# Performance work log

Measured on AMD Instinct MI355X. Metric: run time of the kernel, lower is better.

Reference implementation:

```python
import jax, jax.numpy as jnp
import numpy as np

B, NQ, NK, DQ, DK, H, DV = 4, 128, 1024, 256, 256, 256, 256
MASK_VAL = -1e6


def setup_inputs() -> dict:
    key = jax.random.key(0)
    ks = jax.random.split(key, 7)
    queries = jax.random.normal(ks[0], (B, NQ, DQ), dtype=jnp.float32)
    keys = jax.random.normal(ks[1], (B, NK, DK), dtype=jnp.float32)
    values = jax.random.normal(ks[2], (B, NK, DV), dtype=jnp.float32)
    # per-batch valid lengths in [1, NK]
    valid_lens = jax.random.randint(ks[3], (B,), 1, NK + 1, dtype=jnp.int64 if jax.config.read('jax_enable_x64') else jnp.int32)
    W_q = jax.random.normal(ks[4], (DQ, H), dtype=jnp.float32) * (1.0 / np.sqrt(DQ))
    W_k = jax.random.normal(ks[5], (DK, H), dtype=jnp.float32) * (1.0 / np.sqrt(DK))
    v_w = jax.random.normal(ks[6], (H,), dtype=jnp.float32) * (1.0 / np.sqrt(H))
    return {"queries": queries, "keys": keys, "values": values,
            "valid_lens": valid_lens, "W_q": W_q, "W_k": W_k, "v_w": v_w}


def reference(queries, keys, values, valid_lens, W_q, W_k, v_w):
    # Project queries and keys to the shared hidden space.
    q = jnp.einsum('bqd,dh->bqh', queries, W_q)          # (B, NQ, H)
    k = jnp.einsum('bkd,dh->bkh', keys, W_k)             # (B, NK, H)
    # Broadcast-add + tanh -> (B, NQ, NK, H), then contract with v to scores.
    features = jnp.tanh(q[:, :, None, :] + k[:, None, :, :])
    scores = jnp.einsum('bqkh,h->bqk', features, v_w)    # (B, NQ, NK)
    # Masked softmax over the key axis: positions >= valid_len get -1e6.
    nk = scores.shape[-1]
    mask = jnp.arange(nk)[None, None, :] < valid_lens[:, None, None]
    scores = jnp.where(mask, scores, MASK_VAL)
    attention_weights = jax.nn.softmax(scores, axis=-1)
    # Weighted sum of values (bmm).
    return jnp.einsum('bqk,bkv->bqv', attention_weights, values)
```

## Files before the change

kernel.cpp:

```cpp
#include <hip/hip_runtime.h>

#define B_   4
#define NQ_  128
#define NK_  1024
#define DD_  256
#define H_   256
#define DV_  256

__device__ __forceinline__ float wave_sum(float v) {
  #pragma unroll
  for (int o = 32; o; o >>= 1) v += __shfl_xor(v, o);
  return v;
}
__device__ __forceinline__ float wave_max(float v) {
  #pragma unroll
  for (int o = 32; o; o >>= 1) v = fmaxf(v, __shfl_xor(v, o));
  return v;
}

__global__ __launch_bounds__(256) void proj_merged_kernel(
    const float* __restrict__ queries, const float* __restrict__ keys,
    const float* __restrict__ W_q, const float* __restrict__ W_k,
    float* __restrict__ qp, float* __restrict__ kpT) {
  __shared__ float As[16 * 36];
  __shared__ float Ws[16 * 68];
  __shared__ float Ts[64 * 36];
  const int tid  = threadIdx.x;
  const int row0 = blockIdx.x * 32;
  const int col0 = blockIdx.y * 64;
  const bool isQ = row0 < 512;
  const float* A = isQ ? queries + (size_t)row0 * DD_
                       : keys + (size_t)(row0 - 512) * DD_;
  const float* W = isQ ? W_q : W_k;
  const int ld_d = tid & 15, ld_r = tid >> 4;
  const int lw_n = tid & 63, lw_k = tid >> 6;
  const int tn = tid & 15, tm = tid >> 4;

  float aP[2], wP[4];
  #pragma unroll
  for (int p = 0; p < 2; ++p) aP[p] = A[(size_t)(p * 16 + ld_r) * DD_ + ld_d];
  #pragma unroll
  for (int p = 0; p < 4; ++p) wP[p] = W[(size_t)(p * 4 + lw_k) * H_ + col0 + lw_n];

  float acc[2][4] = {};
  for (int kt = 0; kt < 16; ++kt) {
    __syncthreads();
    #pragma unroll
    for (int p = 0; p < 2; ++p) As[ld_d * 36 + p * 16 + ld_r] = aP[p];
    #pragma unroll
    for (int p = 0; p < 4; ++p) Ws[(p * 4 + lw_k) * 68 + lw_n] = wP[p];
    __syncthreads();
    if (kt < 15) {
      const int k0 = (kt + 1) * 16;
      #pragma unroll
      for (int p = 0; p < 2; ++p) aP[p] = A[(size_t)(p * 16 + ld_r) * DD_ + k0 + ld_d];
      #pragma unroll
      for (int p = 0; p < 4; ++p) wP[p] = W[(size_t)(k0 + p * 4 + lw_k) * H_ + col0 + lw_n];
    }
    #pragma unroll
    for (int kk = 0; kk < 16; ++kk) {
      const float2 a = *(const float2*)&As[kk * 36 + tm * 2];
      const float4 w = *(const float4*)&Ws[kk * 68 + tn * 4];
      acc[0][0] = fmaf(a.x, w.x, acc[0][0]);
      acc[0][1] = fmaf(a.x, w.y, acc[0][1]);
      acc[0][2] = fmaf(a.x, w.z, acc[0][2]);
      acc[0][3] = fmaf(a.x, w.w, acc[0][3]);
      acc[1][0] = fmaf(a.y, w.x, acc[1][0]);
      acc[1][1] = fmaf(a.y, w.y, acc[1][1]);
      acc[1][2] = fmaf(a.y, w.z, acc[1][2]);
      acc[1][3] = fmaf(a.y, w.w, acc[1][3]);
    }
  }

  if (isQ) {
    #pragma unroll
    for (int i = 0; i < 2; ++i) {
      *(float4*)&qp[(size_t)(row0 + tm * 2 + i) * H_ + col0 + tn * 4] =
          make_float4(acc[i][0], acc[i][1], acc[i][2], acc[i][3]);
    }
  } else {
    #pragma unroll
    for (int i = 0; i < 2; ++i)
      #pragma unroll
      for (int j = 0; j < 4; ++j)
        Ts[(tn * 4 + j) * 36 + tm * 2 + i] = acc[i][j];
    __syncthreads();
    const int keyrow = row0 - 512;
    const int b = keyrow >> 10;
    const int kbase = keyrow & (NK_ - 1);
    const int hh = tid >> 2;
    const int kg = (tid & 3) * 8;
    float* dst = kpT + ((size_t)(b * H_ + col0 + hh)) * NK_ + kbase + kg;
    #pragma unroll
    for (int p = 0; p < 2; ++p)
      *(float4*)&dst[p * 4] = *(const float4*)&Ts[hh * 36 + kg + p * 4];
  }
}

__global__ __launch_bounds__(512) void fused_attn_kernel(
    const float* __restrict__ qp, const float* __restrict__ kpT,
    const float* __restrict__ v_w, const float* __restrict__ values,
    const int* __restrict__ valid_lens, float* __restrict__ out) {
  __shared__ float2 qs2[H_];
  __shared__ float w2s[H_];
  __shared__ float reds[4];
  __shared__ float s_half[2][2][NK_];
  __shared__ float redm[2][4];
  __shared__ float redsum[2][4];
  __shared__ float red[8][2][DV_];

  const int tid = threadIdx.x;
  const int n = blockIdx.x;
  const int xcd = n & 7;
  const int b = xcd >> 1;
  const int idx = ((n >> 3) << 1) | (xcd & 1);
  const int qrow = b * NQ_ + idx * 2;

  int vl = valid_lens[b];
  vl = vl < 1 ? 1 : (vl > NK_ ? NK_ : vl);

  const float C2 = 2.8853900817779268f;
  if (tid < H_) {
    const float vw = v_w[tid];
    w2s[tid] = 2.0f * vw;
    const float q0 = qp[(size_t)qrow * H_ + tid];
    const float q1 = qp[(size_t)(qrow + 1) * H_ + tid];
    qs2[tid] = make_float2(q0 * C2, q1 * C2);
    float s = wave_sum(vw);
    if ((tid & 63) == 0) reds[tid >> 6] = s;
  }
  __syncthreads();
  const float wsum = reds[0] + reds[1] + reds[2] + reds[3];

  const int g = tid >> 8;
  const int k0 = (tid & 255) * 4;
  if (k0 < vl) {
    float a0x = 0.f, a0y = 0.f, a0z = 0.f, a0w = 0.f;
    float a1x = 0.f, a1y = 0.f, a1z = 0.f, a1w = 0.f;
    const float* kp = kpT + ((size_t)(b * H_ + g * 128)) * NK_ + k0;
    const float* w2p = w2s + g * 128;
    const float2* q2p = qs2 + g * 128;
    float4 c0 = *(const float4*)(kp + 0 * (size_t)NK_);
    float4 c1 = *(const float4*)(kp + 1 * (size_t)NK_);
    float4 c2 = *(const float4*)(kp + 2 * (size_t)NK_);
    float4 c3 = *(const float4*)(kp + 3 * (size_t)NK_);
#define CONSUME(kv, h)                                                     \
    {                                                                      \
      const float w2 = w2p[h];                                             \
      const float2 q2 = q2p[h];                                            \
      const float e0x = __builtin_amdgcn_exp2f(fmaf((kv).x, C2, q2.x));    \
      const float e0y = __builtin_amdgcn_exp2f(fmaf((kv).y, C2, q2.x));    \
      const float e0z = __builtin_amdgcn_exp2f(fmaf((kv).z, C2, q2.x));    \
      const float e0w = __builtin_amdgcn_exp2f(fmaf((kv).w, C2, q2.x));    \
      const float e1x = __builtin_amdgcn_exp2f(fmaf((kv).x, C2, q2.y));    \
      const float e1y = __builtin_amdgcn_exp2f(fmaf((kv).y, C2, q2.y));    \
      const float e1z = __builtin_amdgcn_exp2f(fmaf((kv).z, C2, q2.y));    \
      const float e1w = __builtin_amdgcn_exp2f(fmaf((kv).w, C2, q2.y));    \
      a0x = fmaf(w2, __builtin_amdgcn_rcpf(1.0f + e0x), a0x);              \
      a0y = fmaf(w2, __builtin_amdgcn_rcpf(1.0f + e0y), a0y);              \
      a0z = fmaf(w2, __builtin_amdgcn_rcpf(1.0f + e0z), a0z);              \
      a0w = fmaf(w2, __builtin_amdgcn_rcpf(1.0f + e0w), a0w);              \
      a1x = fmaf(w2, __builtin_amdgcn_rcpf(1.0f + e1x), a1x);              \
      a1y = fmaf(w2, __builtin_amdgcn_rcpf(1.0f + e1y), a1y);              \
      a1z = fmaf(w2, __builtin_amdgcn_rcpf(1.0f + e1z), a1z);              \
      a1w = fmaf(w2, __builtin_amdgcn_rcpf(1.0f + e1w), a1w);              \
    }
    for (int gg = 0; gg < 31; ++gg) {
      const int hb = gg * 4;
      const float4 n0 = *(const float4*)(kp + (size_t)(hb + 4) * NK_);
      const float4 n1 = *(const float4*)(kp + (size_t)(hb + 5) * NK_);
      const float4 n2 = *(const float4*)(kp + (size_t)(hb + 6) * NK_);
      const float4 n3 = *(const float4*)(kp + (size_t)(hb + 7) * NK_);
      CONSUME(c0, hb + 0)
      CONSUME(c1, hb + 1)
      CONSUME(c2, hb + 2)
      CONSUME(c3, hb + 3)
      c0 = n0; c1 = n1; c2 = n2; c3 = n3;
    }
    CONSUME(c0, 124)
    CONSUME(c1, 125)
    CONSUME(c2, 126)
    CONSUME(c3, 127)
#undef CONSUME
    *(float4*)&s_half[g][0][k0] = make_float4(a0x, a0y, a0z, a0w);
    *(float4*)&s_half[g][1][k0] = make_float4(a1x, a1y, a1z, a1w);
  }
  __syncthreads();

  const int qi = tid >> 8;
  const int k4 = (tid & 255) * 4;
  const float4 pA = *(const float4*)&s_half[0][qi][k4];
  const float4 pB = *(const float4*)&s_half[1][qi][k4];
  const float s0 = wsum - (pA.x + pB.x);
  const float s1 = wsum - (pA.y + pB.y);
  const float s2 = wsum - (pA.z + pB.z);
  const float s3 = wsum - (pA.w + pB.w);
  const float NEG = -3.0e38f;
  float m = NEG;
  m = fmaxf(m, (k4 + 0 < vl) ? s0 : NEG);
  m = fmaxf(m, (k4 + 1 < vl) ? s1 : NEG);
  m = fmaxf(m, (k4 + 2 < vl) ? s2 : NEG);
  m = fmaxf(m, (k4 + 3 < vl) ? s3 : NEG);
  m = wave_max(m);
  if ((tid & 63) == 0) redm[qi][(tid >> 6) & 3] = m;
  __syncthreads();
  const float M = fmaxf(fmaxf(redm[qi][0], redm[qi][1]),
                        fmaxf(redm[qi][2], redm[qi][3]));
  const float CE = 1.4426950408889634f;
  const float p0 = (k4 + 0 < vl) ? __builtin_amdgcn_exp2f((s0 - M) * CE) : 0.0f;
  const float p1 = (k4 + 1 < vl) ? __builtin_amdgcn_exp2f((s1 - M) * CE) : 0.0f;
  const float p2 = (k4 + 2 < vl) ? __builtin_amdgcn_exp2f((s2 - M) * CE) : 0.0f;
  const float p3 = (k4 + 3 < vl) ? __builtin_amdgcn_exp2f((s3 - M) * CE) : 0.0f;
  float psum = wave_sum(p0 + p1 + p2 + p3);
  if ((tid & 63) == 0) redsum[qi][(tid >> 6) & 3] = psum;
  __syncthreads();
  const float S = redsum[qi][0] + redsum[qi][1] + redsum[qi][2] + redsum[qi][3];
  const float inv = 1.0f / S;
  *(float4*)&s_half[0][qi][k4] = make_float4(p0 * inv, p1 * inv, p2 * inv, p3 * inv);
  __syncthreads();

  const int w = tid >> 6;
  const int lane = tid & 63;
  const int d0 = lane * 4;
  float4 pa0 = make_float4(0.f, 0.f, 0.f, 0.f);
  float4 pa1 = make_float4(0.f, 0.f, 0.f, 0.f);
  const int kbeg = w * (NK_ / 8);
  const int kend = (kbeg + NK_ / 8) < vl ? (kbeg + NK_ / 8) : vl;
  const float* vb = values + (size_t)b * NK_ * DV_ + d0;
#define PVSTEP(v4, kk)                                                     \
    {                                                                      \
      const float w0 = s_half[0][0][kk];                                   \
      const float w1 = s_half[0][1][kk];                                   \
      pa0.x = fmaf(w0, (v4).x, pa0.x);                                     \
      pa0.y = fmaf(w0, (v4).y, pa0.y);                                     \
      pa0.z = fmaf(w0, (v4).z, pa0.z);                                     \
      pa0.w = fmaf(w0, (v4).w, pa0.w);                                     \
      pa1.x = fmaf(w1, (v4).x, pa1.x);                                     \
      pa1.y = fmaf(w1, (v4).y, pa1.y);                                     \
      pa1.z = fmaf(w1, (v4).z, pa1.z);                                     \
      pa1.w = fmaf(w1, (v4).w, pa1.w);                                     \
    }
  int k = kbeg;
  if (k + 4 <= kend) {
    float4 v0 = *(const float4*)(vb + (size_t)(k + 0) * DV_);
    float4 v1 = *(const float4*)(vb + (size_t)(k + 1) * DV_);
    float4 v2 = *(const float4*)(vb + (size_t)(k + 2) * DV_);
    float4 v3 = *(const float4*)(vb + (size_t)(k + 3) * DV_);
    for (; k + 8 <= kend; k += 4) {
      const float4 u0 = *(const float4*)(vb + (size_t)(k + 4) * DV_);
      const float4 u1 = *(const float4*)(vb + (size_t)(k + 5) * DV_);
      const float4 u2 = *(const float4*)(vb + (size_t)(k + 6) * DV_);
      const float4 u3 = *(const float4*)(vb + (size_t)(k + 7) * DV_);
      PVSTEP(v0, k + 0)
      PVSTEP(v1, k + 1)
      PVSTEP(v2, k + 2)
      PVSTEP(v3, k + 3)
      v0 = u0; v1 = u1; v2 = u2; v3 = u3;
    }
    PVSTEP(v0, k + 0)
    PVSTEP(v1, k + 1)
    PVSTEP(v2, k + 2)
    PVSTEP(v3, k + 3)
    k += 4;
  }
  for (; k < kend; ++k) {
    const float4 v4 = *(const float4*)(vb + (size_t)k * DV_);
    PVSTEP(v4, k)
  }
#undef PVSTEP
  *(float4*)&red[w][0][d0] = pa0;
  *(float4*)&red[w][1][d0] = pa1;
  __syncthreads();

  const int oqi = tid >> 8;
  const int d = tid & 255;
  float s = 0.f;
  #pragma unroll
  for (int ww = 0; ww < 8; ++ww) s += red[ww][oqi][d];
  out[(size_t)(qrow + oqi) * DV_ + d] = s;
}

extern "C" void kernel_launch(void* const* d_in, const int* in_sizes, int n_in,
                              void* d_out, int out_size, void* d_ws, size_t ws_size,
                              hipStream_t stream) {
  const float* queries = (const float*)d_in[0];
  const float* keys    = (const float*)d_in[1];
  const float* values  = (const float*)d_in[2];
  const int*   vlens   = (const int*)d_in[3];
  const float* W_q     = (const float*)d_in[4];
  const float* W_k     = (const float*)d_in[5];
  const float* v_w     = (const float*)d_in[6];
  float* out = (float*)d_out;

  float* qp  = (float*)d_ws;
  float* kpT = qp + (size_t)B_ * NQ_ * H_;

  proj_merged_kernel<<<dim3((512 + B_ * NK_) / 32, H_ / 64), 256, 0, stream>>>(
      queries, keys, W_q, W_k, qp, kpT);
  fused_attn_kernel<<<(B_ * NQ_) / 2, 512, 0, stream>>>(qp, kpT, v_w, values, vlens, out);
}
```

Before: 123.5 us.

## Process one query per attention block and deepen projection K-tile

```diff
diff --git a/kernel.cpp b/kernel.cpp
--- a/kernel.cpp
+++ b/kernel.cpp
@@ -22,8 +22,8 @@
     const float* __restrict__ queries, const float* __restrict__ keys,
     const float* __restrict__ W_q, const float* __restrict__ W_k,
     float* __restrict__ qp, float* __restrict__ kpT) {
-  __shared__ float As[16 * 36];
-  __shared__ float Ws[16 * 68];
+  __shared__ float As[32 * 36];
+  __shared__ float Ws[32 * 68];
   __shared__ float Ts[64 * 36];
   const int tid  = threadIdx.x;
   const int row0 = blockIdx.x * 32;
@@ -32,33 +32,33 @@
   const float* A = isQ ? queries + (size_t)row0 * DD_
                        : keys + (size_t)(row0 - 512) * DD_;
   const float* W = isQ ? W_q : W_k;
-  const int ld_d = tid & 15, ld_r = tid >> 4;
+  const int ld_d = tid & 31, ld_r = tid >> 5;
   const int lw_n = tid & 63, lw_k = tid >> 6;
   const int tn = tid & 15, tm = tid >> 4;
 
-  float aP[2], wP[4];
-  #pragma unroll
-  for (int p = 0; p < 2; ++p) aP[p] = A[(size_t)(p * 16 + ld_r) * DD_ + ld_d];
-  #pragma unroll
-  for (int p = 0; p < 4; ++p) wP[p] = W[(size_t)(p * 4 + lw_k) * H_ + col0 + lw_n];
+  float aP[4], wP[8];
+  #pragma unroll
+  for (int p = 0; p < 4; ++p) aP[p] = A[(size_t)(p * 8 + ld_r) * DD_ + ld_d];
+  #pragma unroll
+  for (int p = 0; p < 8; ++p) wP[p] = W[(size_t)(p * 4 + lw_k) * H_ + col0 + lw_n];
 
   float acc[2][4] = {};
-  for (int kt = 0; kt < 16; ++kt) {
+  for (int kt = 0; kt < 8; ++kt) {
     __syncthreads();
     #pragma unroll
-    for (int p = 0; p < 2; ++p) As[ld_d * 36 + p * 16 + ld_r] = aP[p];
-    #pragma unroll
-    for (int p = 0; p < 4; ++p) Ws[(p * 4 + lw_k) * 68 + lw_n] = wP[p];
+    for (int p = 0; p < 4; ++p) As[ld_d * 36 + p * 8 + ld_r] = aP[p];
+    #pragma unroll
+    for (int p = 0; p < 8; ++p) Ws[(p * 4 + lw_k) * 68 + lw_n] = wP[p];
     __syncthreads();
-    if (kt < 15) {
-      const int k0 = (kt + 1) * 16;
+    if (kt < 7) {
+      const int k0 = (kt + 1) * 32;
       #pragma unroll
-      for (int p = 0; p < 2; ++p) aP[p] = A[(size_t)(p * 16 + ld_r) * DD_ + k0 + ld_d];
+      for (int p = 0; p < 4; ++p) aP[p] = A[(size_t)(p * 8 + ld_r) * DD_ + k0 + ld_d];
       #pragma unroll
-      for (int p = 0; p < 4; ++p) wP[p] = W[(size_t)(k0 + p * 4 + lw_k) * H_ + col0 + lw_n];
-    }
-    #pragma unroll
-    for (int kk = 0; kk < 16; ++kk) {
+      for (int p = 0; p < 8; ++p) wP[p] = W[(size_t)(k0 + p * 4 + lw_k) * H_ + col0 + lw_n];
+    }
+    #pragma unroll
+    for (int kk = 0; kk < 32; ++kk) {
       const float2 a = *(const float2*)&As[kk * 36 + tm * 2];
       const float4 w = *(const float4*)&Ws[kk * 68 + tn * 4];
       acc[0][0] = fmaf(a.x, w.x, acc[0][0]);
@@ -97,75 +97,61 @@
   }
 }
 
-__global__ __launch_bounds__(512) void fused_attn_kernel(
+__global__ __launch_bounds__(256) void fused_attn_kernel(
     const float* __restrict__ qp, const float* __restrict__ kpT,
     const float* __restrict__ v_w, const float* __restrict__ values,
     const int* __restrict__ valid_lens, float* __restrict__ out) {
-  __shared__ float2 qs2[H_];
+  __shared__ float qs[H_];
   __shared__ float w2s[H_];
   __shared__ float reds[4];
-  __shared__ float s_half[2][2][NK_];
-  __shared__ float redm[2][4];
-  __shared__ float redsum[2][4];
-  __shared__ float red[8][2][DV_];
+  __shared__ float wlds[NK_];
+  __shared__ float redm[4];
+  __shared__ float redsum[4];
+  __shared__ float red[4][DV_];
 
   const int tid = threadIdx.x;
   const int n = blockIdx.x;
   const int xcd = n & 7;
   const int b = xcd >> 1;
   const int idx = ((n >> 3) << 1) | (xcd & 1);
-  const int qrow = b * NQ_ + idx * 2;
+  const int qrow = b * NQ_ + idx;
 
   int vl = valid_lens[b];
   vl = vl < 1 ? 1 : (vl > NK_ ? NK_ : vl);
 
   const float C2 = 2.8853900817779268f;
-  if (tid < H_) {
+  {
     const float vw = v_w[tid];
     w2s[tid] = 2.0f * vw;
-    const float q0 = qp[(size_t)qrow * H_ + tid];
-    const float q1 = qp[(size_t)(qrow + 1) * H_ + tid];
-    qs2[tid] = make_float2(q0 * C2, q1 * C2);
+    qs[tid] = qp[(size_t)qrow * H_ + tid] * C2;
     float s = wave_sum(vw);
     if ((tid & 63) == 0) reds[tid >> 6] = s;
   }
   __syncthreads();
   const float wsum = reds[0] + reds[1] + reds[2] + reds[3];
 
-  const int g = tid >> 8;
-  const int k0 = (tid & 255) * 4;
+  const int k0 = tid * 4;
+  float ax = 0.f, ay = 0.f, az = 0.f, aw = 0.f;
   if (k0 < vl) {
-    float a0x = 0.f, a0y = 0.f, a0z = 0.f, a0w = 0.f;
-    float a1x = 0.f, a1y = 0.f, a1z = 0.f, a1w = 0.f;
-    const float* kp = kpT + ((size_t)(b * H_ + g * 128)) * NK_ + k0;
-    const float* w2p = w2s + g * 128;
-    const float2* q2p = qs2 + g * 128;
+    const float* kp = kpT + ((size_t)(b * H_)) * NK_ + k0;
     float4 c0 = *(const float4*)(kp + 0 * (size_t)NK_);
     float4 c1 = *(const float4*)(kp + 1 * (size_t)NK_);
     float4 c2 = *(const float4*)(kp + 2 * (size_t)NK_);
     float4 c3 = *(const float4*)(kp + 3 * (size_t)NK_);
 #define CONSUME(kv, h)                                                     \
     {                                                                      \
-      const float w2 = w2p[h];                                             \
-      const float2 q2 = q2p[h];                                            \
-      const float e0x = __builtin_amdgcn_exp2f(fmaf((kv).x, C2, q2.x));    \
-      const float e0y = __builtin_amdgcn_exp2f(fmaf((kv).y, C2, q2.x));    \
-      const float e0z = __builtin_amdgcn_exp2f(fmaf((kv).z, C2, q2.x));    \
-      const float e0w = __builtin_amdgcn_exp2f(fmaf((kv).w, C2, q2.x));    \
-      const float e1x = __builtin_amdgcn_exp2f(fmaf((kv).x, C2, q2.y));    \
-      const float e1y = __builtin_amdgcn_exp2f(fmaf((kv).y, C2, q2.y));    \
-      const float e1z = __builtin_amdgcn_exp2f(fmaf((kv).z, C2, q2.y));    \
-      const float e1w = __builtin_amdgcn_exp2f(fmaf((kv).w, C2, q2.y));    \
-      a0x = fmaf(w2, __builtin_amdgcn_rcpf(1.0f + e0x), a0x);              \
-      a0y = fmaf(w2, __builtin_amdgcn_rcpf(1.0f + e0y), a0y);              \
-      a0z = fmaf(w2, __builtin_amdgcn_rcpf(1.0f + e0z), a0z);              \
-      a0w = fmaf(w2, __builtin_amdgcn_rcpf(1.0f + e0w), a0w);              \
-      a1x = fmaf(w2, __builtin_amdgcn_rcpf(1.0f + e1x), a1x);              \
-      a1y = fmaf(w2, __builtin_amdgcn_rcpf(1.0f + e1y), a1y);              \
-      a1z = fmaf(w2, __builtin_amdgcn_rcpf(1.0f + e1z), a1z);              \
-      a1w = fmaf(w2, __builtin_amdgcn_rcpf(1.0f + e1w), a1w);              \
-    }
-    for (int gg = 0; gg < 31; ++gg) {
+      const float w2 = w2s[h];                                             \
+      const float qc = qs[h];                                              \
+      const float ex = __builtin_amdgcn_exp2f(fmaf((kv).x, C2, qc));       \
+      const float ey = __builtin_amdgcn_exp2f(fmaf((kv).y, C2, qc));       \
+      const float ez = __builtin_amdgcn_exp2f(fmaf((kv).z, C2, qc));       \
+      const float ew = __builtin_amdgcn_exp2f(fmaf((kv).w, C2, qc));       \
+      ax = fmaf(w2, __builtin_amdgcn_rcpf(1.0f + ex), ax);                 \
+      ay = fmaf(w2, __builtin_amdgcn_rcpf(1.0f + ey), ay);                 \
+      az = fmaf(w2, __builtin_amdgcn_rcpf(1.0f + ez), az);                 \
+      aw = fmaf(w2, __builtin_amdgcn_rcpf(1.0f + ew), aw);                 \
+    }
+    for (int gg = 0; gg < 63; ++gg) {
       const int hb = gg * 4;
       const float4 n0 = *(const float4*)(kp + (size_t)(hb + 4) * NK_);
       const float4 n1 = *(const float4*)(kp + (size_t)(hb + 5) * NK_);
@@ -177,68 +163,54 @@
       CONSUME(c3, hb + 3)
       c0 = n0; c1 = n1; c2 = n2; c3 = n3;
     }
-    CONSUME(c0, 124)
-    CONSUME(c1, 125)
-    CONSUME(c2, 126)
-    CONSUME(c3, 127)
+    CONSUME(c0, 252)
+    CONSUME(c1, 253)
+    CONSUME(c2, 254)
+    CONSUME(c3, 255)
 #undef CONSUME
-    *(float4*)&s_half[g][0][k0] = make_float4(a0x, a0y, a0z, a0w);
-    *(float4*)&s_half[g][1][k0] = make_float4(a1x, a1y, a1z, a1w);
-  }
-  __syncthreads();
-
-  const int qi = tid >> 8;
-  const int k4 = (tid & 255) * 4;
-  const float4 pA = *(const float4*)&s_half[0][qi][k4];
-  const float4 pB = *(const float4*)&s_half[1][qi][k4];
-  const float s0 = wsum - (pA.x + pB.x);
-  const float s1 = wsum - (pA.y + pB.y);
-  const float s2 = wsum - (pA.z + pB.z);
-  const float s3 = wsum - (pA.w + pB.w);
+  }
+  const float s0 = wsum - ax;
+  const float s1 = wsum - ay;
+  const float s2 = wsum - az;
+  const float s3 = wsum - aw;
+
   const float NEG = -3.0e38f;
   float m = NEG;
-  m = fmaxf(m, (k4 + 0 < vl) ? s0 : NEG);
-  m = fmaxf(m, (k4 + 1 < vl) ? s1 : NEG);
-  m = fmaxf(m, (k4 + 2 < vl) ? s2 : NEG);
-  m = fmaxf(m, (k4 + 3 < vl) ? s3 : NEG);
+  m = fmaxf(m, (k0 + 0 < vl) ? s0 : NEG);
+  m = fmaxf(m, (k0 + 1 < vl) ? s1 : NEG);
+  m = fmaxf(m, (k0 + 2 < vl) ? s2 : NEG);
+  m = fmaxf(m, (k0 + 3 < vl) ? s3 : NEG);
   m = wave_max(m);
-  if ((tid & 63) == 0) redm[qi][(tid >> 6) & 3] = m;
-  __syncthreads();
-  const float M = fmaxf(fmaxf(redm[qi][0], redm[qi][1]),
-                        fmaxf(redm[qi][2], redm[qi][3]));
+  if ((tid & 63) == 0) redm[tid >> 6] = m;
+  __syncthreads();
+  const float M = fmaxf(fmaxf(redm[0], redm[1]), fmaxf(redm[2], redm[3]));
   const float CE = 1.4426950408889634f;
-  const float p0 = (k4 + 0 < vl) ? __builtin_amdgcn_exp2f((s0 - M) * CE) : 0.0f;
-  const float p1 = (k4 + 1 < vl) ? __builtin_amdgcn_exp2f((s1 - M) * CE) : 0.0f;
-  const float p2 = (k4 + 2 < vl) ? __builtin_amdgcn_exp2f((s2 - M) * CE) : 0.0f;
-  const float p3 = (k4 + 3 < vl) ? __builtin_amdgcn_exp2f((s3 - M) * CE) : 0.0f;
+  const float p0 = (k0 + 0 < vl) ? __builtin_amdgcn_exp2f((s0 - M) * CE) : 0.0f;
+  const float p1 = (k0 + 1 < vl) ? __builtin_amdgcn_exp2f((s1 - M) * CE) : 0.0f;
+  const float p2 = (k0 + 2 < vl) ? __builtin_amdgcn_exp2f((s2 - M) * CE) : 0.0f;
+  const float p3 = (k0 + 3 < vl) ? __builtin_amdgcn_exp2f((s3 - M) * CE) : 0.0f;
   float psum = wave_sum(p0 + p1 + p2 + p3);
-  if ((tid & 63) == 0) redsum[qi][(tid >> 6) & 3] = psum;
-  __syncthreads();
-  const float S = redsum[qi][0] + redsum[qi][1] + redsum[qi][2] + redsum[qi][3];
+  if ((tid & 63) == 0) redsum[tid >> 6] = psum;
+  __syncthreads();
+  const float S = redsum[0] + redsum[1] + redsum[2] + redsum[3];
   const float inv = 1.0f / S;
-  *(float4*)&s_half[0][qi][k4] = make_float4(p0 * inv, p1 * inv, p2 * inv, p3 * inv);
+  *(float4*)&wlds[k0] = make_float4(p0 * inv, p1 * inv, p2 * inv, p3 * inv);
   __syncthreads();
 
   const int w = tid >> 6;
   const int lane = tid & 63;
   const int d0 = lane * 4;
-  float4 pa0 = make_float4(0.f, 0.f, 0.f, 0.f);
-  float4 pa1 = make_float4(0.f, 0.f, 0.f, 0.f);
-  const int kbeg = w * (NK_ / 8);
-  const int kend = (kbeg + NK_ / 8) < vl ? (kbeg + NK_ / 8) : vl;
+  float4 pa = make_float4(0.f, 0.f, 0.f, 0.f);
+  const int kbeg = w * (NK_ / 4);
+  const int kend = (kbeg + NK_ / 4) < vl ? (kbeg + NK_ / 4) : vl;
   const float* vb = values + (size_t)b * NK_ * DV_ + d0;
 #define PVSTEP(v4, kk)                                                     \
     {                                                                      \
-      const float w0 = s_half[0][0][kk];                                   \
-      const float w1 = s_half[0][1][kk];                                   \
-      pa0.x = fmaf(w0, (v4).x, pa0.x);                                     \
-      pa0.y = fmaf(w0, (v4).y, pa0.y);                                     \
-      pa0.z = fmaf(w0, (v4).z, pa0.z);                                     \
-      pa0.w = fmaf(w0, (v4).w, pa0.w);                                     \
-      pa1.x = fmaf(w1, (v4).x, pa1.x);                                     \
-      pa1.y = fmaf(w1, (v4).y, pa1.y);                                     \
-      pa1.z = fmaf(w1, (v4).z, pa1.z);                                     \
-      pa1.w = fmaf(w1, (v4).w, pa1.w);                                     \
+      const float w0 = wlds[kk];                                           \
+      pa.x = fmaf(w0, (v4).x, pa.x);                                       \
+      pa.y = fmaf(w0, (v4).y, pa.y);                                       \
+      pa.z = fmaf(w0, (v4).z, pa.z);                                       \
+      pa.w = fmaf(w0, (v4).w, pa.w);                                       \
     }
   int k = kbeg;
   if (k + 4 <= kend) {
@@ -268,16 +240,11 @@
     PVSTEP(v4, k)
   }
 #undef PVSTEP
-  *(float4*)&red[w][0][d0] = pa0;
-  *(float4*)&red[w][1][d0] = pa1;
-  __syncthreads();
-
-  const int oqi = tid >> 8;
-  const int d = tid & 255;
-  float s = 0.f;
-  #pragma unroll
-  for (int ww = 0; ww < 8; ++ww) s += red[ww][oqi][d];
-  out[(size_t)(qrow + oqi) * DV_ + d] = s;
+  *(float4*)&red[w][d0] = pa;
+  __syncthreads();
+
+  const float s = red[0][tid] + red[1][tid] + red[2][tid] + red[3][tid];
+  out[(size_t)qrow * DV_ + tid] = s;
 }
 
 extern "C" void kernel_launch(void* const* d_in, const int* in_sizes, int n_in,
@@ -297,5 +264,5 @@
 
   proj_merged_kernel<<<dim3((512 + B_ * NK_) / 32, H_ / 64), 256, 0, stream>>>(
       queries, keys, W_q, W_k, qp, kpT);
-  fused_attn_kernel<<<(B_ * NQ_) / 2, 512, 0, stream>>>(qp, kpT, v_w, values, vlens, out);
-}
+  fused_attn_kernel<<<B_ * NQ_, 256, 0, stream>>>(qp, kpT, v_w, values, vlens, out);
+}
```

New measurement: 131.2 us. 1.06x slower.
